# Performance work log

Measured on AMD Instinct MI355X. Metric: run time of the kernel, lower is better.

Reference implementation:

```python
import jax, jax.numpy as jnp
import numpy as np


def setup_inputs() -> dict:
    key = jax.random.key(0)
    k1, k2, k3, k4, k5 = jax.random.split(key, 5)
    N, IN, OUT = 4096, 2048, 2048
    return {
        "input": jax.random.normal(k1, (N, IN), dtype=jnp.float32),
        "weight_mu": jax.random.normal(k2, (OUT, IN), dtype=jnp.float32) * 0.25,
        "weight_rho": jax.random.normal(k3, (OUT, IN), dtype=jnp.float32) - 5.0,
        "eps_weight": jax.random.normal(k4, (OUT, IN), dtype=jnp.float32),
        "bias": jax.random.normal(k5, (OUT,), dtype=jnp.float32) * 0.02,
    }


def reference(input, weight_mu, weight_rho, eps_weight, bias):
    # Effective weight: mu + softplus(rho) * eps   (log1p(exp(rho)) == softplus)
    w = weight_mu + jax.nn.softplus(weight_rho) * eps_weight  # [out, in]
    # F.linear: input @ w.T + bias
    return jnp.einsum("ni,oi->no", input, w) + bias
```

## Files before the change

kernel.cpp:

```cpp
#include <hip/hip_runtime.h>
#include <stdint.h>

typedef __bf16 bf16x8 __attribute__((ext_vector_type(8)));
typedef float f32x4 __attribute__((ext_vector_type(4)));
typedef float float4v __attribute__((ext_vector_type(4)));
typedef unsigned short u16x8 __attribute__((ext_vector_type(8)));

__device__ __forceinline__ unsigned short f2bf(float f) {
    unsigned u = __float_as_uint(f);
    u += 0x7fffu + ((u >> 16) & 1u);
    return (unsigned short)(u >> 16);
}

__device__ __forceinline__ float softplus(float x) {
    return fmaxf(x, 0.0f) + __logf(1.0f + __expf(-fabsf(x)));
}

__device__ __forceinline__ void gl_lds16(const void* gptr, void* lptr) {
    auto g = reinterpret_cast<const __attribute__((address_space(1))) void*>(
        reinterpret_cast<uintptr_t>(gptr));
    auto l = reinterpret_cast<__attribute__((address_space(3))) void*>(
        reinterpret_cast<uintptr_t>(lptr));
    __builtin_amdgcn_global_load_lds(g, l, 16, 0, 0);
}

__global__ void prep_kernel(const float* __restrict__ in,
                            const float* __restrict__ mu,
                            const float* __restrict__ rho,
                            const float* __restrict__ eps,
                            unsigned short* __restrict__ in_bf,
                            unsigned short* __restrict__ w_bf,
                            int nIn8, int nW8) {
    int i = blockIdx.x * blockDim.x + threadIdx.x;
    if (i < nIn8) {
        const float4v* p = (const float4v*)in + (size_t)i * 2;
        float4v a = p[0], b = p[1];
        u16x8 r;
        r[0] = f2bf(a[0]); r[1] = f2bf(a[1]); r[2] = f2bf(a[2]); r[3] = f2bf(a[3]);
        r[4] = f2bf(b[0]); r[5] = f2bf(b[1]); r[6] = f2bf(b[2]); r[7] = f2bf(b[3]);
        ((u16x8*)in_bf)[i] = r;
    } else {
        int j = i - nIn8;
        if (j >= nW8) return;
        const float4v* pm = (const float4v*)mu  + (size_t)j * 2;
        const float4v* pr = (const float4v*)rho + (size_t)j * 2;
        const float4v* pe = (const float4v*)eps + (size_t)j * 2;
        float4v m0 = pm[0], m1 = pm[1];
        float4v r0 = pr[0], r1 = pr[1];
        float4v e0 = pe[0], e1 = pe[1];
        u16x8 r;
        r[0] = f2bf(m0[0] + softplus(r0[0]) * e0[0]);
        r[1] = f2bf(m0[1] + softplus(r0[1]) * e0[1]);
        r[2] = f2bf(m0[2] + softplus(r0[2]) * e0[2]);
        r[3] = f2bf(m0[3] + softplus(r0[3]) * e0[3]);
        r[4] = f2bf(m1[0] + softplus(r1[0]) * e1[0]);
        r[5] = f2bf(m1[1] + softplus(r1[1]) * e1[1]);
        r[6] = f2bf(m1[2] + softplus(r1[2]) * e1[2]);
        r[7] = f2bf(m1[3] + softplus(r1[3]) * e1[3]);
        ((u16x8*)w_bf)[j] = r;
    }
}

#define BM 128
#define BN 128
#define BK 64

__global__ __launch_bounds__(512, 4)
void gemm_bt_kernel(const unsigned short* __restrict__ A,
                    const unsigned short* __restrict__ B,
                    const float* __restrict__ bias,
                    float* __restrict__ C,
                    int M, int N, int K) {
    __shared__ unsigned short lds_a[2][BM * BK];
    __shared__ unsigned short lds_b[2][BN * BK];

    const int t      = threadIdx.x;
    const int lane   = t & 63;
    const int wave   = t >> 6;
    const int lane16 = lane & 15;
    const int quad   = lane >> 4;
    const int wm     = wave & 1;
    const int wn     = wave >> 1;

    const int m0 = blockIdx.y * BM;
    const int n0 = blockIdx.x * BN;

    const int r1   = t >> 3;
    const int pkg1 = t & 7;
    const int g1   = (pkg1 ^ (r1 & 7)) * 8;
    const int r2   = r1 + 64;
    const int g2   = (pkg1 ^ (r2 & 7)) * 8;

    const unsigned short* Ab = A + (size_t)m0 * K;
    const unsigned short* Bb = B + (size_t)n0 * K;

    f32x4 acc[4][2] = {};
    const int sw = lane16 & 7;

    auto stage = [&](int buf, int k0) {
        gl_lds16(Ab + (size_t)r1 * K + k0 + g1, &lds_a[buf][t * 8]);
        gl_lds16(Ab + (size_t)r2 * K + k0 + g2, &lds_a[buf][4096 + t * 8]);
        gl_lds16(Bb + (size_t)r1 * K + k0 + g1, &lds_b[buf][t * 8]);
        gl_lds16(Bb + (size_t)r2 * K + k0 + g2, &lds_b[buf][4096 + t * 8]);
    };

    const int nit = K / BK;
    stage(0, 0);
    __syncthreads();

    auto body = [&](int cur, int it) {
        const unsigned short* la = lds_a[cur];
        const unsigned short* lb = lds_b[cur];
        bf16x8 af[2][4], bfr[2][2];
#pragma unroll
        for (int ch = 0; ch < 2; ch++) {
            const int pk = ((ch * 4 + quad) ^ sw) * 8;
#pragma unroll
            for (int mi = 0; mi < 4; mi++)
                af[ch][mi] = *(const bf16x8*)(la + (wm * 64 + mi * 16 + lane16) * BK + pk);
#pragma unroll
            for (int ni = 0; ni < 2; ni++)
                bfr[ch][ni] = *(const bf16x8*)(lb + (wn * 32 + ni * 16 + lane16) * BK + pk);
        }
        if (it + 1 < nit) stage(cur ^ 1, (it + 1) * BK);
#pragma unroll
        for (int ch = 0; ch < 2; ch++)
#pragma unroll
            for (int mi = 0; mi < 4; mi++)
#pragma unroll
                for (int ni = 0; ni < 2; ni++)
                    acc[mi][ni] = __builtin_amdgcn_mfma_f32_16x16x32_bf16(
                        af[ch][mi], bfr[ch][ni], acc[mi][ni], 0, 0, 0);
        __syncthreads();
    };

    for (int it = 0; it < nit; it += 2) {
        body(0, it);
        body(1, it + 1);
    }

    float bv[2];
#pragma unroll
    for (int ni = 0; ni < 2; ni++)
        bv[ni] = bias[n0 + wn * 32 + ni * 16 + lane16];

#pragma unroll
    for (int mi = 0; mi < 4; mi++) {
        const int rbase = m0 + wm * 64 + mi * 16 + quad * 4;
#pragma unroll
        for (int ni = 0; ni < 2; ni++) {
            const int col = n0 + wn * 32 + ni * 16 + lane16;
#pragma unroll
            for (int r = 0; r < 4; r++)
                C[(size_t)(rbase + r) * N + col] = acc[mi][ni][r] + bv[ni];
        }
    }
}

extern "C" void kernel_launch(void* const* d_in, const int* in_sizes, int n_in,
                              void* d_out, int out_size, void* d_ws, size_t ws_size,
                              hipStream_t stream) {
    const float* input = (const float*)d_in[0];
    const float* mu    = (const float*)d_in[1];
    const float* rho   = (const float*)d_in[2];
    const float* eps   = (const float*)d_in[3];
    const float* bias  = (const float*)d_in[4];
    float* out = (float*)d_out;

    const int OUT = in_sizes[4];
    const int IN  = in_sizes[1] / OUT;
    const int M   = in_sizes[0] / IN;

    unsigned short* in_bf = (unsigned short*)d_ws;
    unsigned short* w_bf  = in_bf + (size_t)M * IN;

    const int nIn8 = (M * IN) / 8;
    const int nW8  = (OUT * IN) / 8;
    prep_kernel<<<dim3((nIn8 + nW8 + 255) / 256), 256, 0, stream>>>(
        input, mu, rho, eps, in_bf, w_bf, nIn8, nW8);

    gemm_bt_kernel<<<dim3(OUT / BN, M / BM), 512, 0, stream>>>(
        in_bf, w_bf, bias, out, M, OUT, IN);
}
```

Baseline: 159.8 us.

## Restructure GEMM into a 4-slot LDS ring with 3-deep prefetch and 64x64 wave tiles

The bf16 GEMM changes from 512 threads with a BK=64 double buffer to 256 threads with a 4-slot LDS ring of K=32 chunks. Loads run three chunks ahead, with an explicit vmcnt wait and raw barriers instead of __syncthreads, so more global-to-LDS traffic overlaps the MFMA work. Each wave now computes a 64x64 tile (16 accumulators), which raises register reuse of the A and B fragments, and s_setprio is raised around the MFMA block. In exchange the XOR swizzle on the LDS layout is removed, so fragment reads may hit bank conflicts, and fewer waves per block reduces latency hiding.

```diff
diff --git a/kernel.cpp b/kernel.cpp
--- a/kernel.cpp
+++ b/kernel.cpp
@@ -63,16 +63,16 @@
 
 #define BM 128
 #define BN 128
-#define BK 64
+#define KC 32
+#define SLOT_U 8192
 
-__global__ __launch_bounds__(512, 4)
+__global__ __launch_bounds__(256, 2)
 void gemm_bt_kernel(const unsigned short* __restrict__ A,
                     const unsigned short* __restrict__ B,
                     const float* __restrict__ bias,
                     float* __restrict__ C,
                     int M, int N, int K) {
-    __shared__ unsigned short lds_a[2][BM * BK];
-    __shared__ unsigned short lds_b[2][BN * BK];
+    __shared__ unsigned short lds[4][SLOT_U];
 
     const int t      = threadIdx.x;
     const int lane   = t & 63;
@@ -85,74 +85,74 @@
     const int m0 = blockIdx.y * BM;
     const int n0 = blockIdx.x * BN;
 
-    const int r1   = t >> 3;
-    const int pkg1 = t & 7;
-    const int g1   = (pkg1 ^ (r1 & 7)) * 8;
-    const int r2   = r1 + 64;
-    const int g2   = (pkg1 ^ (r2 & 7)) * 8;
+    const int r  = t >> 2;
+    const int kg = (t & 3) * 8;
 
-    const unsigned short* Ab = A + (size_t)m0 * K;
-    const unsigned short* Bb = B + (size_t)n0 * K;
+    const unsigned short* a0 = A + (size_t)(m0 + r)      * K + kg;
+    const unsigned short* a1 = A + (size_t)(m0 + 64 + r) * K + kg;
+    const unsigned short* b0 = B + (size_t)(n0 + r)      * K + kg;
+    const unsigned short* b1 = B + (size_t)(n0 + 64 + r) * K + kg;
 
-    f32x4 acc[4][2] = {};
-    const int sw = lane16 & 7;
+    f32x4 acc[4][4] = {};
 
-    auto stage = [&](int buf, int k0) {
-        gl_lds16(Ab + (size_t)r1 * K + k0 + g1, &lds_a[buf][t * 8]);
-        gl_lds16(Ab + (size_t)r2 * K + k0 + g2, &lds_a[buf][4096 + t * 8]);
-        gl_lds16(Bb + (size_t)r1 * K + k0 + g1, &lds_b[buf][t * 8]);
-        gl_lds16(Bb + (size_t)r2 * K + k0 + g2, &lds_b[buf][4096 + t * 8]);
+    auto stage = [&](int slot, int kc) {
+        const int k0 = kc * KC;
+        gl_lds16(a0 + k0, &lds[slot][t * 8]);
+        gl_lds16(a1 + k0, &lds[slot][2048 + t * 8]);
+        gl_lds16(b0 + k0, &lds[slot][4096 + t * 8]);
+        gl_lds16(b1 + k0, &lds[slot][6144 + t * 8]);
     };
 
-    const int nit = K / BK;
+    const int nchunk = K / KC;
     stage(0, 0);
-    __syncthreads();
+    stage(1, 1);
+    stage(2, 2);
 
-    auto body = [&](int cur, int it) {
-        const unsigned short* la = lds_a[cur];
-        const unsigned short* lb = lds_b[cur];
-        bf16x8 af[2][4], bfr[2][2];
+    const int ra = (wm * 64 + lane16) * KC + quad * 8;
+    const int rb = 4096 + (wn * 64 + lane16) * KC + quad * 8;
+
+#pragma unroll 4
+    for (int i = 0; i < nchunk; ++i) {
+        const int slot = i & 3;
+        stage((i + 3) & 3, (i + 3 < nchunk) ? (i + 3) : (nchunk - 1));
+        asm volatile("s_waitcnt vmcnt(12)" ::: "memory");
+        __builtin_amdgcn_sched_barrier(0);
+        __builtin_amdgcn_s_barrier();
+        const unsigned short* ls = lds[slot];
+        bf16x8 af[4], bf[4];
 #pragma unroll
-        for (int ch = 0; ch < 2; ch++) {
-            const int pk = ((ch * 4 + quad) ^ sw) * 8;
+        for (int mi = 0; mi < 4; ++mi)
+            af[mi] = *(const bf16x8*)(ls + ra + mi * 16 * KC);
 #pragma unroll
-            for (int mi = 0; mi < 4; mi++)
-                af[ch][mi] = *(const bf16x8*)(la + (wm * 64 + mi * 16 + lane16) * BK + pk);
+        for (int ni = 0; ni < 4; ++ni)
+            bf[ni] = *(const bf16x8*)(ls + rb + ni * 16 * KC);
+        __builtin_amdgcn_s_setprio(1);
 #pragma unroll
-            for (int ni = 0; ni < 2; ni++)
-                bfr[ch][ni] = *(const bf16x8*)(lb + (wn * 32 + ni * 16 + lane16) * BK + pk);
-        }
-        if (it + 1 < nit) stage(cur ^ 1, (it + 1) * BK);
+        for (int mi = 0; mi < 4; ++mi)
 #pragma unroll
-        for (int ch = 0; ch < 2; ch++)
-#pragma unroll
-            for (int mi = 0; mi < 4; mi++)
-#pragma unroll
-                for (int ni = 0; ni < 2; ni++)
-                    acc[mi][ni] = __builtin_amdgcn_mfma_f32_16x16x32_bf16(
-                        af[ch][mi], bfr[ch][ni], acc[mi][ni], 0, 0, 0);
-        __syncthreads();
-    };
-
-    for (int it = 0; it < nit; it += 2) {
-        body(0, it);
-        body(1, it + 1);
+            for (int ni = 0; ni < 4; ++ni)
+                acc[mi][ni] = __builtin_amdgcn_mfma_f32_16x16x32_bf16(
+                    af[mi], bf[ni], acc[mi][ni], 0, 0, 0);
+        __builtin_amdgcn_s_setprio(0);
+        asm volatile("s_waitcnt lgkmcnt(0)" ::: "memory");
+        __builtin_amdgcn_sched_barrier(0);
+        __builtin_amdgcn_s_barrier();
     }
 
-    float bv[2];
+    float bv[4];
 #pragma unroll
-    for (int ni = 0; ni < 2; ni++)
-        bv[ni] = bias[n0 + wn * 32 + ni * 16 + lane16];
+    for (int ni = 0; ni < 4; ++ni)
+        bv[ni] = bias[n0 + wn * 64 + ni * 16 + lane16];
 
 #pragma unroll
-    for (int mi = 0; mi < 4; mi++) {
+    for (int mi = 0; mi < 4; ++mi) {
         const int rbase = m0 + wm * 64 + mi * 16 + quad * 4;
 #pragma unroll
-        for (int ni = 0; ni < 2; ni++) {
-            const int col = n0 + wn * 32 + ni * 16 + lane16;
+        for (int ni = 0; ni < 4; ++ni) {
+            const int col = n0 + wn * 64 + ni * 16 + lane16;
 #pragma unroll
-            for (int r = 0; r < 4; r++)
-                C[(size_t)(rbase + r) * N + col] = acc[mi][ni][r] + bv[ni];
+            for (int rr = 0; rr < 4; ++rr)
+                C[(size_t)(rbase + rr) * N + col] = acc[mi][ni][rr] + bv[ni];
         }
     }
 }
@@ -179,6 +179,6 @@
     prep_kernel<<<dim3((nIn8 + nW8 + 255) / 256), 256, 0, stream>>>(
         input, mu, rho, eps, in_bf, w_bf, nIn8, nW8);
 
-    gemm_bt_kernel<<<dim3(OUT / BN, M / BM), 512, 0, stream>>>(
+    gemm_bt_kernel<<<dim3(OUT / BN, M / BM), 256, 0, stream>>>(
         in_bf, w_bf, bias, out, M, OUT, IN);
 }
```

New measurement: 165.6 us. 3.6% more time.
